# Optimization experiments

Measured on AMD Instinct MI355X. Metric: run time of the kernel, lower is better.

The kernel has to match this reference:

```python
import jax, jax.numpy as jnp
import numpy as np

B, C, H, W = 16, 3, 128, 128
PATCH = 8
E = 512          # embedding_dim
NH = 8           # num_heads
P = 64           # proj_dim
HID = 2048       # hidden_dim
L = 6            # num_layers
COND = 3
PH, PW = H // PATCH, W // PATCH
S = PH * PW + 1  # sequence length (patches + cond token)
INV_SQRT_E = 1.0 / np.float32(np.sqrt(E))

_PARAM_SHAPES = {
    'patch_w': (E, C, PATCH, PATCH), 'patch_b': (E,),
    'cond_w1': (COND, E), 'cond_b1': (E,), 'cond_w2': (E, E), 'cond_b2': (E,),
    'pos_embed': (1, S, E),
    'enc_vp': (L, NH, E, P), 'enc_kp': (L, NH, E, P), 'enc_qh': (L, NH, S, S), 'enc_lift': (L, 1, NH * P, E),
    'enc_ln1g': (L, E), 'enc_ln1b': (L, E),
    'enc_w1': (L, E, HID), 'enc_b1': (L, HID), 'enc_w2': (L, HID, E), 'enc_b2': (L, E),
    'enc_ln2g': (L, E), 'enc_ln2b': (L, E),
    'dec_vp': (L, NH, E, P), 'dec_kp': (L, NH, E, P), 'dec_qh': (L, NH, S, S), 'dec_lift': (L, 1, NH * P, E),
    'dec_ln2g': (L, E), 'dec_ln2b': (L, E),
    'dec_w1': (L, E, HID), 'dec_b1': (L, HID), 'dec_w2': (L, HID, E), 'dec_b2': (L, E),
    'dec_ln3g': (L, E), 'dec_ln3b': (L, E),
    'final_g': (E,), 'final_b': (E,),
    'deconv_w': (E, C, PATCH, PATCH), 'deconv_b': (C,),
}


def setup_inputs() -> dict:
    key = jax.random.key(0)
    inp = {
        'x': jax.random.normal(jax.random.fold_in(key, 1000), (B, C, H, W), jnp.float32),
        'y': jax.random.normal(jax.random.fold_in(key, 1001), (B, COND), jnp.float32),
    }
    for i, (name, shp) in enumerate(_PARAM_SHAPES.items()):
        w = 0.02 * jax.random.normal(jax.random.fold_in(key, i), shp, jnp.float32)
        if name.endswith('g'):  # layernorm gains near 1
            w = w + 1.0
        inp[name] = w
    return inp


def _ln(x, g, b, eps=1e-5):
    m = x.mean(-1, keepdims=True)
    v = ((x - m) ** 2).mean(-1, keepdims=True)
    return (x - m) * jax.lax.rsqrt(v + eps) * g + b


def _mhsa(x, vp, kp, qh, lift):
    # x: (B,S,E); vp/kp: (NH,E,P); qh: (NH,S,S); lift: (1, NH*P, E)
    k = jnp.einsum('bse,hep->bhsp', x, kp)
    v = jnp.einsum('bse,hep->bhsp', x, vp)
    qv = jnp.einsum('hst,bhtp->bhsp', qh, v)
    # a_ts = (qh@V) @ K^T, then transpose(-2,-1): a[t,s] = qv[s] . k[t]
    a = jnp.einsum('bhsp,bhtp->bhts', qv, k) * INV_SQRT_E
    a = jax.nn.softmax(a, axis=-1)
    o = jnp.einsum('bhst,bhtp->bhsp', a, v)          # (B,NH,S,P)
    o = o.transpose(0, 2, 1, 3).reshape(x.shape[0], S, NH * P)
    return o @ lift[0]


def _block(z, vp, kp, qh, lift, g1, b1, w1, fb1, w2, fb2, g2, b2):
    z = _ln(z + _mhsa(z, vp, kp, qh, lift), g1, b1)
    h = jax.nn.leaky_relu(z @ w1 + fb1, 0.2) @ w2 + fb2  # dropout = identity (eval)
    return _ln(z + h, g2, b2)


def reference(x, y, patch_w, patch_b, cond_w1, cond_b1, cond_w2, cond_b2, pos_embed,
              enc_vp, enc_kp, enc_qh, enc_lift, enc_ln1g, enc_ln1b,
              enc_w1, enc_b1, enc_w2, enc_b2, enc_ln2g, enc_ln2b,
              dec_vp, dec_kp, dec_qh, dec_lift, dec_ln2g, dec_ln2b,
              dec_w1, dec_b1, dec_w2, dec_b2, dec_ln3g, dec_ln3b,
              final_g, final_b, deconv_w, deconv_b):
    b = x.shape[0]
    # Patching: Conv2d(k=p, s=p) == block-reshape + einsum
    xp = x.reshape(b, C, PH, PATCH, PW, PATCH)
    tok = jnp.einsum('bchpwq,ecpq->bhwe', xp, patch_w).reshape(b, PH * PW, E) + patch_b
    cond = jax.nn.leaky_relu(y @ cond_w1 + cond_b1, 0.2)
    cond = jax.nn.leaky_relu(cond @ cond_w2 + cond_b2, 0.2)
    z = jnp.concatenate([cond[:, None, :], tok], axis=1) + pos_embed
    for i in range(L):
        z = _block(z, enc_vp[i], enc_kp[i], enc_qh[i], enc_lift[i],
                   enc_ln1g[i], enc_ln1b[i], enc_w1[i], enc_b1[i],
                   enc_w2[i], enc_b2[i], enc_ln2g[i], enc_ln2b[i])
    for i in range(L):  # decoder: only mhsa_2 / ln2 / ff / ln3 are used
        z = _block(z, dec_vp[i], dec_kp[i], dec_qh[i], dec_lift[i],
                   dec_ln2g[i], dec_ln2b[i], dec_w1[i], dec_b1[i],
                   dec_w2[i], dec_b2[i], dec_ln3g[i], dec_ln3b[i])
    z = _ln(z[:, 1:], final_g, final_b)               # drop cond token
    g = z.reshape(b, PH, PW, E)                        # (B,E,PH,PW) grid, channels-last form
    out = jnp.einsum('bhwe,ecpq->bchpwq', g, deconv_w).reshape(b, C, H, W)
    return out + deconv_b[None, :, None, None]
```

## Files before the change

### kernel.cpp

```cpp
#include <hip/hip_runtime.h>
#include <stdint.h>
#include <math.h>

#define B_    16
#define C_    3
#define HIMG  128
#define E_    512
#define NH_   8
#define S_    257
#define T_    256
#define MTOK  4096
#define MSEQ  4112
#define HID_  2048
#define SP_   288
#define SLAB  (288*288)
#define PS    2105344L
#define INV_SQRT_E 0.044194173824159216f

typedef __attribute__((ext_vector_type(8))) __bf16 bf16x8;
typedef __attribute__((ext_vector_type(4))) float f32x4;

__device__ __forceinline__ void gload16(const void* g, const void* lds)
{
    __builtin_amdgcn_global_load_lds(
        (const __attribute__((address_space(1))) uint32_t*)(uintptr_t)g,
        (__attribute__((address_space(3))) uint32_t*)(uint32_t)(uintptr_t)lds,
        16, 0, 0);
}

template<int WMW, int WNW, bool LEAKY, bool OUTF32, bool VSPLIT>
__device__ __forceinline__ void gemm_core(
    const __bf16* __restrict__ A, int lda,
    const __bf16* __restrict__ Bt, int ldb,
    void* __restrict__ C, int ldc,
    const float* __restrict__ bias, float scale,
    int M, int N, int K, int tm, int tn, __bf16* __restrict__ vTout)
{
    constexpr int BM  = WMW * 64;
    constexpr int BN  = WNW * 32;
    constexpr int T   = WMW * WNW * 64;
    constexpr int ACH = BM * 4;
    constexpr int BCH = BN * 4;
    constexpr int LPT = ACH / T + BCH / T;
    __shared__ __align__(16) __bf16 sA[4][BM * 32];
    __shared__ __align__(16) __bf16 sB[4][BN * 32];

    const int tid  = threadIdx.x;
    const int lane = tid & 63;
    const int wid  = tid >> 6;
    const int wm   = wid / WNW;
    const int wn   = wid % WNW;
    const int lh   = lane >> 4;
    const int ll   = lane & 15;

    const __bf16* Ab = A + (long)tm * BM * lda;
    const __bf16* Bb = Bt + (long)tn * BN * ldb;

    f32x4 acc[4][2] = {};
    const int nst = K >> 5;

    auto stage = [&](int buf, int k0) {
#pragma unroll
        for (int rr = 0; rr < ACH / T; ++rr) {
            const int L = rr * T + tid;
            const int row = L >> 2;
            const int gch = (L & 3) ^ ((row >> 1) & 3);
            gload16(Ab + (long)row * lda + k0 + gch * 8,
                    (const char*)(&sA[buf][0]) + (rr * T + (wid << 6)) * 16);
        }
#pragma unroll
        for (int rr = 0; rr < BCH / T; ++rr) {
            const int L = rr * T + tid;
            const int row = L >> 2;
            const int gch = (L & 3) ^ ((row >> 1) & 3);
            gload16(Bb + (long)row * ldb + k0 + gch * 8,
                    (const char*)(&sB[buf][0]) + (rr * T + (wid << 6)) * 16);
        }
    };

    const int PF = nst < 3 ? nst : 3;
    for (int s = 0; s < PF; ++s) stage(s & 3, s << 5);

    for (int st = 0; st < nst; ++st) {
        const int rem = nst - 1 - st;
        if (rem >= 2)      asm volatile("s_waitcnt vmcnt(%0)" :: "n"(2 * LPT) : "memory");
        else if (rem == 1) asm volatile("s_waitcnt vmcnt(%0)" :: "n"(LPT) : "memory");
        else               asm volatile("s_waitcnt vmcnt(0)" ::: "memory");
        __builtin_amdgcn_s_barrier();
        __builtin_amdgcn_sched_barrier(0);

        if (st + 3 < nst) stage((st + 3) & 3, (st + 3) << 5);

        const int cur = st & 3;
        bf16x8 afr[4], bfr[2];
#pragma unroll
        for (int i = 0; i < 4; ++i) {
            const int rw = wm * 64 + i * 16 + ll;
            const int c  = lh ^ ((rw >> 1) & 3);
            afr[i] = *reinterpret_cast<const bf16x8*>(&sA[cur][rw * 32 + c * 8]);
        }
#pragma unroll
        for (int j = 0; j < 2; ++j) {
            const int rw = wn * 32 + j * 16 + ll;
            const int c  = lh ^ ((rw >> 1) & 3);
            bfr[j] = *reinterpret_cast<const bf16x8*>(&sB[cur][rw * 32 + c * 8]);
        }
#pragma unroll
        for (int i = 0; i < 4; ++i)
#pragma unroll
            for (int j = 0; j < 2; ++j)
                acc[i][j] = __builtin_amdgcn_mfma_f32_16x16x32_bf16(
                                afr[i], bfr[j], acc[i][j], 0, 0, 0);
    }

#pragma unroll
    for (int i = 0; i < 4; ++i)
#pragma unroll
        for (int ii = 0; ii < 4; ++ii) {
            const int m = tm * BM + wm * 64 + i * 16 + lh * 4 + ii;
            if (m >= M) continue;
#pragma unroll
            for (int j = 0; j < 2; ++j) {
                const int n = tn * BN + wn * 32 + j * 16 + ll;
                if (n >= N) continue;
                float v = acc[i][j][ii] * scale;
                if (bias) v += bias[n];
                if (LEAKY) v = v > 0.f ? v : 0.2f * v;
                if (VSPLIT && n >= 512) {
                    const int b = m / S_;
                    const int t = m - b * S_;
                    const int hp = n - 512;
                    vTout[(((long)(b * 8 + (hp >> 6)) * 64) + (hp & 63)) * SP_ + t] =
                        (__bf16)v;
                } else if (OUTF32) {
                    ((float*)C)[(long)m * ldc + n] = v;
                } else {
                    ((__bf16*)C)[(long)m * ldc + n] = (__bf16)v;
                }
            }
        }
}

__device__ __forceinline__ int xcd_swizzle(int wg, int nwg)
{
    const int q = nwg >> 3, r = nwg & 7;
    if (q == 0) return wg;
    const int xcd = wg & 7, off = wg >> 3;
    return (xcd < r ? xcd * (q + 1) : r * (q + 1) + (xcd - r) * q) + off;
}

template<int WMW, int WNW, bool LEAKY, bool OUTF32, bool VSPLIT>
__global__ __launch_bounds__(WMW * WNW * 64) void gemm_k(
    const __bf16* __restrict__ A, int lda, const __bf16* __restrict__ Bt, int ldb,
    void* __restrict__ C, int ldc, const float* __restrict__ bias, float scale,
    int M, int N, int K, int ntn, __bf16* __restrict__ vTout)
{
    const int wg = xcd_swizzle(blockIdx.x, gridDim.x);
    gemm_core<WMW, WNW, LEAKY, OUTF32, VSPLIT>(A, lda, Bt, ldb, C, ldc, bias, scale,
                                               M, N, K, wg / ntn, wg % ntn, vTout);
}

template<int WMW, int WNW>
__global__ __launch_bounds__(WMW * WNW * 64) void gemm_split_k(
    const __bf16* __restrict__ A, int lda, const __bf16* __restrict__ Bt, int ldb,
    __bf16* __restrict__ P, long pstride, const float* __restrict__ bias,
    int M, int N, int K, int npart, int ntn)
{
    const int part = blockIdx.y;
    const int Kp = K / npart;
    const int wg = xcd_swizzle(blockIdx.x, gridDim.x);
    gemm_core<WMW, WNW, false, false, false>(A + (long)part * Kp, lda,
                                             Bt + (long)part * Kp, ldb,
                                             P + (long)part * pstride, N,
                                             part == 0 ? bias : nullptr, 1.f,
                                             M, N, Kp, wg / ntn, wg % ntn, nullptr);
}

__global__ __launch_bounds__(256) void qv_k(const __bf16* __restrict__ qhb,
                                            const __bf16* __restrict__ vT,
                                            __bf16* __restrict__ qvcat)
{
    const int bh = blockIdx.z, b = bh >> 3, h = bh & 7;
    gemm_core<2, 2, false, false, false>(qhb + (long)h * SLAB, SP_,
                                         vT + (long)bh * 64 * SP_, SP_,
                                         qvcat + (long)b * S_ * E_ + h * 64, E_,
                                         nullptr, 1.f, S_, 64, SP_, blockIdx.x, 0,
                                         nullptr);
}

__global__ __launch_bounds__(256) void fa_k(const __bf16* __restrict__ kcat,
                                            const __bf16* __restrict__ qvcat,
                                            const __bf16* __restrict__ vT,
                                            __bf16* __restrict__ ocat)
{
    __shared__ __align__(16) __bf16 sK[64 * 64], sQV[64 * 64], sV[64 * 64];
    __shared__ __align__(16) __bf16 sP[4][16 * 64];
    const int bh = blockIdx.y, b = bh >> 3, h = bh & 7;
    const int i0 = blockIdx.x * 64;
    const int tid = threadIdx.x, lane = tid & 63, wid = tid >> 6;
    const int ll = lane & 15, lh = lane >> 4;

    const __bf16* kSrc = kcat + ((long)(b * S_ + i0)) * 512 + h * 64;
    const __bf16* qvB  = qvcat + (long)b * S_ * E_ + h * 64;
    const __bf16* vTb  = vT + (long)bh * 64 * SP_;

    auto stage64 = [&](__bf16* lds, const __bf16* src, int ldsrc) {
#pragma unroll
        for (int r = 0; r < 2; ++r) {
            const int L = r * 256 + wid * 64 + lane;
            const int row = L >> 3, c = L & 7;
            const int sc = c ^ (row & 7);
            gload16(src + (long)row * ldsrc + sc * 8,
                    (const char*)lds + (r * 256 + wid * 64) * 16);
        }
    };

    stage64(sK, kSrc, 512);
    stage64(sQV, qvB, E_);
    stage64(sV, vTb, SP_);
    __syncthreads();

    bf16x8 ka[2];
#pragma unroll
    for (int ks = 0; ks < 2; ++ks) {
        const int row = wid * 16 + ll;
        ka[ks] = *reinterpret_cast<const bf16x8*>(
            &sK[row * 64 + (((ks * 4 + lh) ^ (row & 7)) << 3)]);
    }

    float m[4], l[4];
#pragma unroll
    for (int ii = 0; ii < 4; ++ii) { m[ii] = -1e30f; l[ii] = 0.f; }
    f32x4 oacc[4] = {};

    for (int jt = 0; jt < 5; ++jt) {
        const int j0 = jt * 64;
        f32x4 s[4] = {};
#pragma unroll
        for (int ks = 0; ks < 2; ++ks)
#pragma unroll
            for (int nf = 0; nf < 4; ++nf) {
                const int row = nf * 16 + ll;
                const bf16x8 qb = *reinterpret_cast<const bf16x8*>(
                    &sQV[row * 64 + (((ks * 4 + lh) ^ (row & 7)) << 3)]);
                s[nf] = __builtin_amdgcn_mfma_f32_16x16x32_bf16(ka[ks], qb, s[nf], 0, 0, 0);
            }
        float pv[4][4];
#pragma unroll
        for (int ii = 0; ii < 4; ++ii) {
            float mx = -1e30f;
#pragma unroll
            for (int nf = 0; nf < 4; ++nf) {
                float sv = s[nf][ii] * INV_SQRT_E;
                if (j0 + nf * 16 + ll >= S_) sv = -1e30f;
                pv[nf][ii] = sv;
                mx = fmaxf(mx, sv);
            }
#pragma unroll
            for (int msk = 1; msk < 16; msk <<= 1) mx = fmaxf(mx, __shfl_xor(mx, msk));
            const float mnew = fmaxf(m[ii], mx);
            const float resc = __expf(m[ii] - mnew);
            m[ii] = mnew;
            float sum = 0.f;
#pragma unroll
            for (int nf = 0; nf < 4; ++nf) {
                const float e = __expf(pv[nf][ii] - mnew);
                pv[nf][ii] = e; sum += e;
            }
#pragma unroll
            for (int msk = 1; msk < 16; msk <<= 1) sum += __shfl_xor(sum, msk);
            l[ii] = l[ii] * resc + sum;
#pragma unroll
            for (int pf = 0; pf < 4; ++pf) oacc[pf][ii] *= resc;
        }
        __bf16* sPw = &sP[wid][0];
#pragma unroll
        for (int nf = 0; nf < 4; ++nf)
#pragma unroll
            for (int ii = 0; ii < 4; ++ii) {
                const int row = lh * 4 + ii, col = ll + 16 * nf;
                sPw[row * 64 + ((((col >> 3) ^ (row & 7)) << 3) | (col & 7))] =
                    (__bf16)pv[nf][ii];
            }
#pragma unroll
        for (int ks = 0; ks < 2; ++ks) {
            const bf16x8 pa = *reinterpret_cast<const bf16x8*>(
                &sPw[ll * 64 + (((ks * 4 + lh) ^ (ll & 7)) << 3)]);
#pragma unroll
            for (int pf = 0; pf < 4; ++pf) {
                const int row = pf * 16 + ll;
                const bf16x8 vb = *reinterpret_cast<const bf16x8*>(
                    &sV[row * 64 + (((ks * 4 + lh) ^ (row & 7)) << 3)]);
                oacc[pf] = __builtin_amdgcn_mfma_f32_16x16x32_bf16(pa, vb, oacc[pf], 0, 0, 0);
            }
        }
        if (jt < 4) {
            __syncthreads();
            stage64(sQV, qvB + (long)(j0 + 64) * E_, E_);
            stage64(sV, vTb + j0 + 64, SP_);
            __syncthreads();
        }
    }
#pragma unroll
    for (int ii = 0; ii < 4; ++ii) {
        const int i = i0 + wid * 16 + lh * 4 + ii;
        if (i >= S_) continue;
        const float invl = 1.f / l[ii];
#pragma unroll
        for (int pf = 0; pf < 4; ++pf)
            ocat[((long)(b * S_ + i)) * E_ + h * 64 + pf * 16 + ll] =
                (__bf16)(oacc[pf][ii] * invl);
    }
}

__global__ void ln_kernel(const __bf16* x,
                          const __bf16* __restrict__ parts, int nparts, long pstride,
                          const float* __restrict__ g, const float* __restrict__ bb,
                          __bf16* outb, int skip_cond, int nrows)
{
    const int row = blockIdx.x * 4 + (threadIdx.x >> 6);
    if (row >= nrows) return;
    const int lane = threadIdx.x & 63;
    const long xrow = skip_cond ? (long)row + (row >> 8) + 1 : (long)row;
    const bf16x8 xa = *reinterpret_cast<const bf16x8*>(x + xrow * E_ + lane * 8);
    float e[8];
#pragma unroll
    for (int i = 0; i < 8; ++i) e[i] = (float)xa[i];
    for (int p = 0; p < nparts; ++p) {
        const bf16x8 pv = *reinterpret_cast<const bf16x8*>(
            parts + (long)p * pstride + (long)row * E_ + lane * 8);
#pragma unroll
        for (int i = 0; i < 8; ++i) e[i] += (float)pv[i];
    }
    float s = 0.f;
#pragma unroll
    for (int i = 0; i < 8; ++i) s += e[i];
#pragma unroll
    for (int o = 32; o; o >>= 1) s += __shfl_xor(s, o);
    const float mean = s * (1.f / 512.f);
    float v = 0.f;
#pragma unroll
    for (int i = 0; i < 8; ++i) { e[i] -= mean; v += e[i] * e[i]; }
#pragma unroll
    for (int o = 32; o; o >>= 1) v += __shfl_xor(v, o);
    const float inv = rsqrtf(v * (1.f / 512.f) + 1e-5f);
    const float4* gp = (const float4*)g + lane * 2;
    const float4* bp = (const float4*)bb + lane * 2;
    const float4 g0 = gp[0], g1 = gp[1], bb0 = bp[0], bb1 = bp[1];
    const float gv[8] = {g0.x, g0.y, g0.z, g0.w, g1.x, g1.y, g1.z, g1.w};
    const float bv[8] = {bb0.x, bb0.y, bb0.z, bb0.w, bb1.x, bb1.y, bb1.z, bb1.w};
    bf16x8 ov;
#pragma unroll
    for (int i = 0; i < 8; ++i) ov[i] = (__bf16)(e[i] * inv * gv[i] + bv[i]);
    *reinterpret_cast<bf16x8*>(outb + (long)row * E_ + lane * 8) = ov;
}

__global__ void conv_straight(const float* __restrict__ in, __bf16* __restrict__ out, long n)
{
    const long i = (long)blockIdx.x * 256 + threadIdx.x;
    if (i < n) out[i] = (__bf16)in[i];
}

__global__ void conv_transpose(const float* __restrict__ in, __bf16* __restrict__ out,
                               int R, int C)
{
    __shared__ float tile[32][33];
    const int r0 = blockIdx.x * 32, c0 = blockIdx.y * 32;
    const int tx = threadIdx.x & 31, ty = threadIdx.x >> 5;
#pragma unroll
    for (int i = 0; i < 32; i += 8) {
        const int rr = r0 + ty + i, cc = c0 + tx;
        tile[ty + i][tx] = (rr < R && cc < C) ? in[(long)rr * C + cc] : 0.f;
    }
    __syncthreads();
#pragma unroll
    for (int i = 0; i < 32; i += 8) {
        const int cc = c0 + ty + i, rr = r0 + tx;
        if (cc < C && rr < R) out[(long)cc * R + rr] = (__bf16)tile[tx][ty + i];
    }
}

__global__ void wconv_all(const float* __restrict__ enc_kp, const float* __restrict__ dec_kp,
                          const float* __restrict__ enc_vp, const float* __restrict__ dec_vp,
                          const float* __restrict__ enc_lift, const float* __restrict__ dec_lift,
                          const float* __restrict__ enc_w1, const float* __restrict__ dec_w1,
                          const float* __restrict__ enc_w2, const float* __restrict__ dec_w2,
                          __bf16* __restrict__ kvT, __bf16* __restrict__ liftT,
                          __bf16* __restrict__ w1T, __bf16* __restrict__ w2T)
{
    const int lyr = blockIdx.z;
    const bool enc = lyr < 6;
    const int li = enc ? lyr : lyr - 6;
    const int j = blockIdx.y;
    const float* src; __bf16* dst; int R, C, nb;
    switch (j) {
        case 0:  src = (enc ? enc_kp : dec_kp) + (long)li * 262144;
                 dst = kvT + (long)lyr * 524288;            R = 512; C = 64;   nb = 8; break;
        case 1:  src = (enc ? enc_vp : dec_vp) + (long)li * 262144;
                 dst = kvT + (long)lyr * 524288 + 262144;   R = 512; C = 64;   nb = 8; break;
        case 2:  src = (enc ? enc_lift : dec_lift) + (long)li * 262144;
                 dst = liftT + (long)lyr * 262144;          R = 512; C = 512;  nb = 1; break;
        case 3:  src = (enc ? enc_w1 : dec_w1) + (long)li * 1048576;
                 dst = w1T + (long)lyr * 1048576;           R = 512; C = 2048; nb = 1; break;
        default: src = (enc ? enc_w2 : dec_w2) + (long)li * 1048576;
                 dst = w2T + (long)lyr * 1048576;           R = 2048; C = 512; nb = 1; break;
    }
    const int tR = R >> 5, tC = C >> 5;
    int t = blockIdx.x;
    if (t >= tR * tC * nb) return;
    const int bt = t / (tR * tC);
    t %= tR * tC;
    const int rt = t / tC, ct = t % tC;
    const long bs = (long)R * C;
    const float* ip = src + (long)bt * bs;
    __bf16* op = dst + (long)bt * bs;
    __shared__ float tile[32][33];
    const int tx = threadIdx.x & 31, ty = threadIdx.x >> 5;
#pragma unroll
    for (int i = 0; i < 32; i += 8)
        tile[ty + i][tx] = ip[(long)(rt * 32 + ty + i) * C + ct * 32 + tx];
    __syncthreads();
#pragma unroll
    for (int i = 0; i < 32; i += 8)
        op[(long)(ct * 32 + ty + i) * R + rt * 32 + tx] = (__bf16)tile[tx][ty + i];
}

__global__ void conv_qh_all(const float* __restrict__ enc_qh,
                            const float* __restrict__ dec_qh,
                            __bf16* __restrict__ out)
{
    const long n = 12L * 8 * SLAB;
    for (long o = (long)blockIdx.x * 256 + threadIdx.x; o < n; o += (long)gridDim.x * 256) {
        const int t = (int)(o % SP_);
        const long rr = o / SP_;
        const int s = (int)(rr % SP_);
        const long hh = rr / SP_;
        const int h = (int)(hh % 8);
        const int lyr = (int)(hh / 8);
        float v = 0.f;
        if (s < S_ && t < S_) {
            const float* src = (lyr < 6 ? enc_qh + (long)lyr * 8 * S_ * S_
                                        : dec_qh + (long)(lyr - 6) * 8 * S_ * S_);
            v = src[((long)h * S_ + s) * S_ + t];
        }
        out[o] = (__bf16)v;
    }
}

__global__ void vpad_kernel(__bf16* __restrict__ vT)
{
    const int i = blockIdx.x * 256 + threadIdx.x;
    if (i >= 128 * 64 * 31) return;
    const int t = 257 + (i % 31);
    const long rp = i / 31;
    vT[rp * SP_ + t] = (__bf16)0.f;
}

__global__ void im2col_kernel(const float* __restrict__ x, __bf16* __restrict__ xcol)
{
    const int idx = blockIdx.x * 256 + threadIdx.x;
    if (idx >= MTOK * 192) return;
    const int m = idx / 192, k = idx % 192;
    const int b = m >> 8, t = m & 255;
    const int ph = t >> 4, pw = t & 15;
    const int c = k >> 6, rr = k & 63;
    const int p = rr >> 3, q = rr & 7;
    xcol[idx] = (__bf16)x[(((long)(b * C_ + c) * HIMG) + ph * 8 + p) * HIMG + pw * 8 + q];
}

__global__ void cond_kernel(const float* __restrict__ y,
                            const float* __restrict__ w1, const float* __restrict__ b1,
                            const float* __restrict__ w2, const float* __restrict__ b2,
                            const float* __restrict__ pos, __bf16* __restrict__ zb)
{
    __shared__ float c1[512];
    const int b = blockIdx.x;
    const int e = threadIdx.x;
    float v = y[b * 3 + 0] * w1[e] + y[b * 3 + 1] * w1[512 + e]
            + y[b * 3 + 2] * w1[1024 + e] + b1[e];
    v = v > 0.f ? v : 0.2f * v;
    c1[e] = v;
    __syncthreads();
    float acc = b2[e];
    for (int k = 0; k < 512; ++k) acc += c1[k] * w2[k * 512 + e];
    acc = acc > 0.f ? acc : 0.2f * acc;
    zb[(long)b * S_ * E_ + e] = (__bf16)(acc + pos[e]);
}

__global__ void assemble_kernel(const __bf16* __restrict__ tok,
                                const float* __restrict__ pos,
                                __bf16* __restrict__ zb)
{
    const int idx = blockIdx.x * 256 + threadIdx.x;
    if (idx >= MTOK * E_) return;
    const int m = idx >> 9;
    const int e = idx & 511;
    const int b = m >> 8, t = m & 255;
    const float o = (float)tok[idx] + pos[(1 + t) * E_ + e];
    zb[((long)b * S_ + 1 + t) * E_ + e] = (__bf16)o;
}

__global__ void scatter_kernel(const float* __restrict__ dtmp,
                               const float* __restrict__ db,
                               float* __restrict__ out)
{
    const int idx = blockIdx.x * 256 + threadIdx.x;
    if (idx >= B_ * C_ * HIMG * HIMG) return;
    const int b  = idx / (C_ * HIMG * HIMG);
    const int rm = idx % (C_ * HIMG * HIMG);
    const int c  = rm / (HIMG * HIMG);
    const int hh = (rm % (HIMG * HIMG)) / HIMG;
    const int ww = rm % HIMG;
    const int ph = hh >> 3, p = hh & 7;
    const int pw = ww >> 3, q = ww & 7;
    out[idx] = dtmp[((long)(b * 256 + ph * 16 + pw)) * 192 + c * 64 + p * 8 + q] + db[c];
}

extern "C" void kernel_launch(void* const* d_in, const int* in_sizes, int n_in,
                              void* d_out, int out_size, void* d_ws, size_t ws_size,
                              hipStream_t stream)
{
    const float* x        = (const float*)d_in[0];
    const float* y        = (const float*)d_in[1];
    const float* patch_w  = (const float*)d_in[2];
    const float* patch_b  = (const float*)d_in[3];
    const float* cond_w1  = (const float*)d_in[4];
    const float* cond_b1  = (const float*)d_in[5];
    const float* cond_w2  = (const float*)d_in[6];
    const float* cond_b2  = (const float*)d_in[7];
    const float* pos      = (const float*)d_in[8];
    const float* enc_vp   = (const float*)d_in[9];
    const float* enc_kp   = (const float*)d_in[10];
    const float* enc_qh   = (const float*)d_in[11];
    const float* enc_lift = (const float*)d_in[12];
    const float* enc_ln1g = (const float*)d_in[13];
    const float* enc_ln1b = (const float*)d_in[14];
    const float* enc_w1   = (const float*)d_in[15];
    const float* enc_b1   = (const float*)d_in[16];
    const float* enc_w2   = (const float*)d_in[17];
    const float* enc_b2   = (const float*)d_in[18];
    const float* enc_ln2g = (const float*)d_in[19];
    const float* enc_ln2b = (const float*)d_in[20];
    const float* dec_vp   = (const float*)d_in[21];
    const float* dec_kp   = (const float*)d_in[22];
    const float* dec_qh   = (const float*)d_in[23];
    const float* dec_lift = (const float*)d_in[24];
    const float* dec_ln2g = (const float*)d_in[25];
    const float* dec_ln2b = (const float*)d_in[26];
    const float* dec_w1   = (const float*)d_in[27];
    const float* dec_b1   = (const float*)d_in[28];
    const float* dec_w2   = (const float*)d_in[29];
    const float* dec_b2   = (const float*)d_in[30];
    const float* dec_ln3g = (const float*)d_in[31];
    const float* dec_ln3b = (const float*)d_in[32];
    const float* final_g  = (const float*)d_in[33];
    const float* final_b  = (const float*)d_in[34];
    const float* deconv_w = (const float*)d_in[35];
    const float* deconv_b = (const float*)d_in[36];
    float* out = (float*)d_out;

    char* wp = (char*)d_ws;
    auto alloc_f32 = [&](long n) { float* p = (float*)wp; wp += ((n * 4 + 63) & ~63LL); return p; };
    auto alloc_bf  = [&](long n) { __bf16* p = (__bf16*)wp; wp += ((n * 2 + 63) & ~63LL); return p; };

    float*  dtmp   = alloc_f32(786432);
    __bf16* zb     = alloc_bf(4352L * 512);
    __bf16* tok    = alloc_bf(4096L * 512);
    __bf16* xcolb  = alloc_bf(786432);
    __bf16* kcat   = alloc_bf(4352L * 512);
    __bf16* qvcat  = alloc_bf(4352L * 512);
    __bf16* ocat   = alloc_bf(4352L * 512);
    __bf16* vT     = alloc_bf(128L * 64 * SP_);
    __bf16* psl    = alloc_bf(4L * PS);
    __bf16* hidden = alloc_bf(4224L * 2048);
    __bf16* gbuf   = alloc_bf(4096L * 512);
    __bf16* pwb    = alloc_bf(512L * 192);
    __bf16* dwTb   = alloc_bf(192L * 512);
    __bf16* kvT12  = alloc_bf(12L * 524288);
    __bf16* liftT12= alloc_bf(12L * 262144);
    __bf16* w1T12  = alloc_bf(12L * 1048576);
    __bf16* w2T12  = alloc_bf(12L * 1048576);
    __bf16* qhb12  = alloc_bf(12L * 8 * SLAB + 96L * SP_);
    (void)ws_size; (void)in_sizes; (void)n_in; (void)out_size;

    const dim3 blk(256);

    conv_straight<<<dim3(384), blk, 0, stream>>>(patch_w, pwb, 98304);
    conv_transpose<<<dim3(16, 6), blk, 0, stream>>>(deconv_w, dwTb, 512, 192);
    wconv_all<<<dim3(1024, 5, 12), blk, 0, stream>>>(
        enc_kp, dec_kp, enc_vp, dec_vp, enc_lift, dec_lift,
        enc_w1, dec_w1, enc_w2, dec_w2, kvT12, liftT12, w1T12, w2T12);
    conv_qh_all<<<dim3(4096), blk, 0, stream>>>(enc_qh, dec_qh, qhb12);
    vpad_kernel<<<dim3(992), blk, 0, stream>>>(vT);

    im2col_kernel<<<dim3(3072), blk, 0, stream>>>(x, xcolb);
    gemm_k<2, 2, false, false, false><<<dim3(256), blk, 0, stream>>>(
        xcolb, 192, pwb, 192, tok, 512, patch_b, 1.f, MTOK, 512, 192, 8, nullptr);
    cond_kernel<<<dim3(B_), dim3(512), 0, stream>>>(y, cond_w1, cond_b1,
                                                    cond_w2, cond_b2, pos, zb);
    assemble_kernel<<<dim3(8192), blk, 0, stream>>>(tok, pos, zb);

    for (int l = 0; l < 12; ++l) {
        const bool enc = l < 6;
        const int  li  = enc ? l : l - 6;
        const float* g1   = (enc ? enc_ln1g : dec_ln2g) + li * E_;
        const float* bb1  = (enc ? enc_ln1b : dec_ln2b) + li * E_;
        const float* fb1  = (enc ? enc_b1   : dec_b1)   + li * HID_;
        const float* fb2  = (enc ? enc_b2   : dec_b2)   + li * E_;
        const float* g2   = (enc ? enc_ln2g : dec_ln3g) + li * E_;
        const float* bb2  = (enc ? enc_ln2b : dec_ln3b) + li * E_;
        const __bf16* kvTb   = kvT12 + (long)l * 524288;
        const __bf16* liftTb = liftT12 + (long)l * 262144;
        const __bf16* w1Tb   = w1T12 + (long)l * 1048576;
        const __bf16* w2Tb   = w2T12 + (long)l * 1048576;
        const __bf16* qhb    = qhb12 + (long)l * 8 * SLAB;

        gemm_k<2, 2, false, false, true><<<dim3(528), blk, 0, stream>>>(
            zb, 512, kvTb, 512, kcat, 512, nullptr, 1.f, MSEQ, 1024, 512, 16, vT);
        qv_k<<<dim3(3, 1, 128), blk, 0, stream>>>(qhb, vT, qvcat);
        fa_k<<<dim3(5, 128), blk, 0, stream>>>(kcat, qvcat, vT, ocat);
        gemm_split_k<2, 2><<<dim3(264, 2), blk, 0, stream>>>(
            ocat, 512, liftTb, 512, psl, PS, nullptr, MSEQ, 512, 512, 2, 8);
        ln_kernel<<<dim3(1028), blk, 0, stream>>>(zb, psl, 2, PS, g1, bb1,
                                                  zb, 0, MSEQ);

        gemm_k<2, 2, true, false, false><<<dim3(1056), blk, 0, stream>>>(
            zb, 512, w1Tb, 512, hidden, 2048, fb1, 1.f, MSEQ, HID_, 512, 32, nullptr);
        gemm_split_k<2, 2><<<dim3(264, 4), blk, 0, stream>>>(
            hidden, 2048, w2Tb, 2048, psl, PS, fb2, MSEQ, 512, HID_, 4, 8);
        ln_kernel<<<dim3(1028), blk, 0, stream>>>(zb, psl, 4, PS, g2, bb2,
                                                  zb, 0, MSEQ);
    }

    ln_kernel<<<dim3(1024), blk, 0, stream>>>(zb, nullptr, 0, 0, final_g, final_b,
                                              gbuf, 1, MTOK);
    gemm_k<2, 2, false, true, false><<<dim3(96), blk, 0, stream>>>(
        gbuf, 512, dwTb, 512, dtmp, 192, nullptr, 1.f, MTOK, 192, 512, 3, nullptr);
    scatter_kernel<<<dim3(3072), blk, 0, stream>>>(dtmp, deconv_b, out);
}
```

Baseline: 1.527 ms.

## Double-buffer attention tiles, add MFMA priority hints, widen weight transpose, halve FF2 split-K

The attention kernel now double-buffers the QV and V tiles, so the next tile is staged while the current one is computed, which removes one of the two barriers per iteration. s_setprio hints are placed around the MFMA blocks in both the GEMM core and the attention kernel. The weight transpose/convert kernel now works on 64x64 tiles with float4 loads and bf16x8 stores. The second feed-forward GEMM uses split-K of 2 instead of 4, which reduces partial-sum traffic for the layernorm but exposes less parallelism.

After: 1.499 ms. Within noise of the previous version (-1.8%).

```diff
diff --git a/kernel.cpp b/kernel.cpp
--- a/kernel.cpp
+++ b/kernel.cpp
@@ -105,12 +105,14 @@
             const int c  = lh ^ ((rw >> 1) & 3);
             bfr[j] = *reinterpret_cast<const bf16x8*>(&sB[cur][rw * 32 + c * 8]);
         }
+        __builtin_amdgcn_s_setprio(1);
 #pragma unroll
         for (int i = 0; i < 4; ++i)
 #pragma unroll
             for (int j = 0; j < 2; ++j)
                 acc[i][j] = __builtin_amdgcn_mfma_f32_16x16x32_bf16(
                                 afr[i], bfr[j], acc[i][j], 0, 0, 0);
+        __builtin_amdgcn_s_setprio(0);
     }
 
 #pragma unroll
@@ -193,7 +195,7 @@
                                             const __bf16* __restrict__ vT,
                                             __bf16* __restrict__ ocat)
 {
-    __shared__ __align__(16) __bf16 sK[64 * 64], sQV[64 * 64], sV[64 * 64];
+    __shared__ __align__(16) __bf16 sK[64 * 64], sQV[2][64 * 64], sV[2][64 * 64];
     __shared__ __align__(16) __bf16 sP[4][16 * 64];
     const int bh = blockIdx.y, b = bh >> 3, h = bh & 7;
     const int i0 = blockIdx.x * 64;
@@ -216,8 +218,8 @@
     };
 
     stage64(sK, kSrc, 512);
-    stage64(sQV, qvB, E_);
-    stage64(sV, vTb, SP_);
+    stage64(sQV[0], qvB, E_);
+    stage64(sV[0], vTb, SP_);
     __syncthreads();
 
     bf16x8 ka[2];
@@ -235,16 +237,23 @@
 
     for (int jt = 0; jt < 5; ++jt) {
         const int j0 = jt * 64;
+        const int cur = jt & 1;
+        if (jt < 4) {
+            stage64(sQV[cur ^ 1], qvB + (long)(j0 + 64) * E_, E_);
+            stage64(sV[cur ^ 1], vTb + j0 + 64, SP_);
+        }
         f32x4 s[4] = {};
+        __builtin_amdgcn_s_setprio(1);
 #pragma unroll
         for (int ks = 0; ks < 2; ++ks)
 #pragma unroll
             for (int nf = 0; nf < 4; ++nf) {
                 const int row = nf * 16 + ll;
                 const bf16x8 qb = *reinterpret_cast<const bf16x8*>(
-                    &sQV[row * 64 + (((ks * 4 + lh) ^ (row & 7)) << 3)]);
+                    &sQV[cur][row * 64 + (((ks * 4 + lh) ^ (row & 7)) << 3)]);
                 s[nf] = __builtin_amdgcn_mfma_f32_16x16x32_bf16(ka[ks], qb, s[nf], 0, 0, 0);
             }
+        __builtin_amdgcn_s_setprio(0);
         float pv[4][4];
 #pragma unroll
         for (int ii = 0; ii < 4; ++ii) {
@@ -282,6 +291,7 @@
                 sPw[row * 64 + ((((col >> 3) ^ (row & 7)) << 3) | (col & 7))] =
                     (__bf16)pv[nf][ii];
             }
+        __builtin_amdgcn_s_setprio(1);
 #pragma unroll
         for (int ks = 0; ks < 2; ++ks) {
             const bf16x8 pa = *reinterpret_cast<const bf16x8*>(
@@ -290,16 +300,12 @@
             for (int pf = 0; pf < 4; ++pf) {
                 const int row = pf * 16 + ll;
                 const bf16x8 vb = *reinterpret_cast<const bf16x8*>(
-                    &sV[row * 64 + (((ks * 4 + lh) ^ (row & 7)) << 3)]);
+                    &sV[cur][row * 64 + (((ks * 4 + lh) ^ (row & 7)) << 3)]);
                 oacc[pf] = __builtin_amdgcn_mfma_f32_16x16x32_bf16(pa, vb, oacc[pf], 0, 0, 0);
             }
         }
-        if (jt < 4) {
-            __syncthreads();
-            stage64(sQV, qvB + (long)(j0 + 64) * E_, E_);
-            stage64(sV, vTb + j0 + 64, SP_);
-            __syncthreads();
-        }
+        __builtin_amdgcn_s_setprio(0);
+        if (jt < 4) __syncthreads();
     }
 #pragma unroll
     for (int ii = 0; ii < 4; ++ii) {
@@ -405,7 +411,7 @@
         default: src = (enc ? enc_w2 : dec_w2) + (long)li * 1048576;
                  dst = w2T + (long)lyr * 1048576;           R = 2048; C = 512; nb = 1; break;
     }
-    const int tR = R >> 5, tC = C >> 5;
+    const int tR = R >> 6, tC = C >> 6;
     int t = blockIdx.x;
     if (t >= tR * tC * nb) return;
     const int bt = t / (tR * tC);
@@ -414,15 +420,29 @@
     const long bs = (long)R * C;
     const float* ip = src + (long)bt * bs;
     __bf16* op = dst + (long)bt * bs;
-    __shared__ float tile[32][33];
-    const int tx = threadIdx.x & 31, ty = threadIdx.x >> 5;
-#pragma unroll
-    for (int i = 0; i < 32; i += 8)
-        tile[ty + i][tx] = ip[(long)(rt * 32 + ty + i) * C + ct * 32 + tx];
+    __shared__ float tile[64][65];
+    const int tx4 = (threadIdx.x & 15) * 4;
+    const int tyr = threadIdx.x >> 4;
+#pragma unroll
+    for (int i = 0; i < 64; i += 16) {
+        const float4 v4 = *reinterpret_cast<const float4*>(
+            &ip[(long)(rt * 64 + tyr + i) * C + ct * 64 + tx4]);
+        tile[tyr + i][tx4]     = v4.x;
+        tile[tyr + i][tx4 + 1] = v4.y;
+        tile[tyr + i][tx4 + 2] = v4.z;
+        tile[tyr + i][tx4 + 3] = v4.w;
+    }
     __syncthreads();
-#pragma unroll
-    for (int i = 0; i < 32; i += 8)
-        op[(long)(ct * 32 + ty + i) * R + rt * 32 + tx] = (__bf16)tile[tx][ty + i];
+    const int cw = threadIdx.x >> 3;
+    const int r0 = (threadIdx.x & 7) * 8;
+#pragma unroll
+    for (int pass = 0; pass < 2; ++pass) {
+        const int c = pass * 32 + cw;
+        bf16x8 v;
+#pragma unroll
+        for (int k = 0; k < 8; ++k) v[k] = (__bf16)tile[r0 + k][c];
+        *reinterpret_cast<bf16x8*>(&op[(long)(ct * 64 + c) * R + rt * 64 + r0]) = v;
+    }
 }
 
 __global__ void conv_qh_all(const float* __restrict__ enc_qh,
@@ -587,7 +607,7 @@
 
     conv_straight<<<dim3(384), blk, 0, stream>>>(patch_w, pwb, 98304);
     conv_transpose<<<dim3(16, 6), blk, 0, stream>>>(deconv_w, dwTb, 512, 192);
-    wconv_all<<<dim3(1024, 5, 12), blk, 0, stream>>>(
+    wconv_all<<<dim3(256, 5, 12), blk, 0, stream>>>(
         enc_kp, dec_kp, enc_vp, dec_vp, enc_lift, dec_lift,
         enc_w1, dec_w1, enc_w2, dec_w2, kvT12, liftT12, w1T12, w2T12);
     conv_qh_all<<<dim3(4096), blk, 0, stream>>>(enc_qh, dec_qh, qhb12);
@@ -626,9 +646,9 @@
 
         gemm_k<2, 2, true, false, false><<<dim3(1056), blk, 0, stream>>>(
             zb, 512, w1Tb, 512, hidden, 2048, fb1, 1.f, MSEQ, HID_, 512, 32, nullptr);
-        gemm_split_k<2, 2><<<dim3(264, 4), blk, 0, stream>>>(
-            hidden, 2048, w2Tb, 2048, psl, PS, fb2, MSEQ, 512, HID_, 4, 8);
-        ln_kernel<<<dim3(1028), blk, 0, stream>>>(zb, psl, 4, PS, g2, bb2,
+        gemm_split_k<2, 2><<<dim3(264, 2), blk, 0, stream>>>(
+            hidden, 2048, w2Tb, 2048, psl, PS, fb2, MSEQ, 512, HID_, 2, 8);
+        ln_kernel<<<dim3(1028), blk, 0, stream>>>(zb, psl, 2, PS, g2, bb2,
                                                   zb, 0, MSEQ);
     }
 
```
